# Kernel optimization log

Hardware: AMD Instinct MI355X
Metric: run time of the kernel (lower is better)

The kernel has to match this reference:

```python
import jax, jax.numpy as jnp
import numpy as np

B, T, D = 1, 256, 80
CC = 256        # conv_channels
CCEP = 222      # ccep_size
K = 3           # kernel_size
FFT = 1024
HOP = 256
WIN = 512       # window_size = 2*hop
PF_K = 128      # ltv_postfilter_kernel_size


def conv1d_same(x, w, b, dilation=1):
    """x: (B, L, Cin), w: (Cout, Cin, K) -> (B, L, Cout), 'same' padding."""
    k = w.shape[-1]
    ke = (k - 1) * dilation + 1
    pad = ((ke - 1) // 2, ke - 1 - (ke - 1) // 2)
    y = jax.lax.conv_general_dilated(
        x, w, window_strides=(1,), padding=[pad], rhs_dilation=(dilation,),
        dimension_numbers=('NWC', 'OIW', 'NWC'))
    return y + b


def setup_inputs() -> dict:
    key = jax.random.key(0)
    ks = jax.random.split(key, 8)
    def mkw(k, o, i, kk, scale=1.0):
        return (jax.random.normal(k, (o, i, kk), jnp.float32) * scale / np.sqrt(i * kk)).astype(jnp.float32)
    x = jax.random.normal(ks[0], (B, T, D), jnp.float32)
    z = jax.random.normal(ks[1], (B, 1, T * HOP), jnp.float32)
    w1 = mkw(ks[2], CC, D, K);    b1 = jnp.zeros((CC,), jnp.float32)
    w2 = mkw(ks[3], CC, CC, K);   b2 = jnp.zeros((CC,), jnp.float32)
    w3 = mkw(ks[4], CCEP, CC, K, 0.1); b3 = jnp.zeros((CCEP,), jnp.float32)
    pf_w = mkw(ks[5], 1, 1, PF_K); pf_b = jnp.zeros((1,), jnp.float32)
    # quefrency norm buffer: cat(flip(1..111), 1..111)
    idx = jnp.arange(1, CCEP // 2 + 1, dtype=jnp.float32)
    quef_norm = jnp.concatenate([idx[::-1], idx])
    win = 0.5 * (1.0 - jnp.cos(2.0 * jnp.pi * jnp.arange(WIN, dtype=jnp.float32) / WIN))
    return dict(x=x, z=z, w1=w1, b1=b1, w2=w2, b2=b2, w3=w3, b3=b3,
                pf_w=pf_w, pf_b=pf_b, quef_norm=quef_norm, win=win)


def reference(x, z, w1, b1, w2, b2, w3, b3, pf_w, pf_b, quef_norm, win):
    # --- ConvLayers front-end: conv stack producing complex cepstrum per frame ---
    h = jax.nn.relu(conv1d_same(x, w1, b1))
    h = jax.nn.relu(conv1d_same(h, w2, b2))
    ccep = conv1d_same(h, w3, b3) / quef_norm           # (B, T, 222)
    # --- _ccep2impulse: pad -> FFT -> exp10(mag), keep phase -> IFFT.real ---
    pad = (FFT - CCEP) // 2
    cc = jnp.pad(ccep, ((0, 0), (0, 0), (pad, pad)))    # (B, T, 1024)
    Y = jnp.fft.fft(cc, n=FFT, axis=-1)
    mag = jnp.power(10.0, Y.real / 10.0)
    phase = Y.imag
    imp = jnp.fft.ifft(mag * jnp.cos(phase) + 1j * (mag * jnp.sin(phase)),
                       n=FFT, axis=-1).real.astype(jnp.float32)  # (B, T, 1024)
    # --- _conv_impulse: double unfold + per-frame matmul ---
    zp = jnp.pad(z, ((0, 0), (0, 0), (WIN // 2 - 1, WIN // 2)))      # (B,1,L+511)
    fidx = jnp.arange(T)[:, None] * HOP + jnp.arange(WIN)[None, :]   # (T, 512)
    frames = zp[:, :, fidx]                                          # (B,1,T,512)
    fp = jnp.pad(frames, ((0, 0), (0, 0), (0, 0), (FFT // 2 - 1, FFT // 2)))  # (B,1,T,1535)
    widx = jnp.arange(WIN)[:, None] + jnp.arange(FFT)[None, :]       # (512, 1024)
    wins = fp[:, :, :, widx]                                         # (B,1,T,512,1024)
    out = jnp.einsum('bctwk,btk->bctw', wins, imp)                   # (B,1,T,512)
    # --- _ola: window, split, roll-add, flatten ---
    out = out * win
    l, r = out[..., :HOP], out[..., HOP:]
    s = (l + jnp.roll(r, 1, axis=2)).reshape(B, 1, T * HOP)          # (B,1,L)
    # --- ltv postfilter: 1-ch conv1d (channels-last, 'same') ---
    y = conv1d_same(jnp.transpose(s, (0, 2, 1)), pf_w, pf_b)
    return jnp.transpose(y, (0, 2, 1))
```

## Files before the change

kernel.cpp:

```cpp
#include <hip/hip_runtime.h>

#define T_FRAMES 256
#define D_IN 80
#define CCH 256
#define CCEP 222
#define FFT_N 1024
#define HOP 256
#define WINL 512
#define PF_KT 128
#define ZLEN 65536

__device__ __forceinline__ unsigned br10(unsigned x) { return __brev(x) >> 22; }

__device__ __forceinline__ void conv_inner(const float4* __restrict__ wlds4,
                                           const float4* __restrict__ inlds4,
                                           int c, int fh, float* __restrict__ acc) {
  #pragma unroll
  for (int cg = 0; cg < 4; ++cg) {
    float4 w0 = wlds4[(cg * 3 + 0) * 256 + c];
    float4 w1v = wlds4[(cg * 3 + 1) * 256 + c];
    float4 w2v = wlds4[(cg * 3 + 2) * 256 + c];
    float4 xr[10];
    #pragma unroll
    for (int r = 0; r < 10; ++r) xr[r] = inlds4[(fh * 8 + r) * 4 + cg];
    #pragma unroll
    for (int j = 0; j < 8; ++j) {
      float4 xa = xr[j], xb = xr[j + 1], xc = xr[j + 2];
      acc[j] += xa.x * w0.x  + xb.x * w0.y  + xc.x * w0.z
              + xa.y * w0.w  + xb.y * w1v.x + xc.y * w1v.y
              + xa.z * w1v.z + xb.z * w1v.w + xc.z * w2v.x
              + xa.w * w2v.y + xb.w * w2v.z + xc.w * w2v.w;
    }
  }
}

__global__ __launch_bounds__(512) void conv12_k(const float* __restrict__ x, const float* __restrict__ w1,
                                                const float* __restrict__ b1, const float* __restrict__ w2,
                                                float* __restrict__ h2p) {
  __shared__ float4 wlds4[12 * 256];
  __shared__ float  w1lds[240 * 16];
  __shared__ float4 xlds4[20 * 20];
  __shared__ float4 inlds4[18 * 4];
  const int kc = blockIdx.x, g = blockIdx.y, tid = threadIdx.x;
  const int t0 = g << 4;
  const float4* w24 = (const float4*)w2;
  const float4* x4 = (const float4*)x;
  #pragma unroll
  for (int it = 0; it < 6; ++it) {
    int idx = it * 512 + tid, cc = idx & 255, j4 = idx >> 8;
    wlds4[j4 * 256 + cc] = w24[cc * 192 + kc * 12 + j4];
  }
  for (int idx = tid; idx < 3840; idx += 512) {
    int ch = idx & 15, j = idx >> 4;
    w1lds[j * 16 + ch] = w1[(kc * 16 + ch) * 240 + j];
  }
  if (tid < 400) {
    int f = tid / 20, cg = tid - f * 20;
    int tt = t0 - 2 + f;
    xlds4[f * 20 + cg] = (tt >= 0 && tt < T_FRAMES) ? x4[tt * 20 + cg] : make_float4(0.f, 0.f, 0.f, 0.f);
  }
  __syncthreads();
  if (tid < 288) {
    int f = tid >> 4, ch = tid & 15;
    int tt = t0 - 1 + f;
    float acc = b1[kc * 16 + ch];
    const float* x0 = (const float*)&xlds4[(f + 0) * 20];
    const float* x1 = (const float*)&xlds4[(f + 1) * 20];
    const float* x2 = (const float*)&xlds4[(f + 2) * 20];
    #pragma unroll 8
    for (int cin = 0; cin < D_IN; ++cin) {
      acc += x0[cin] * w1lds[(cin * 3 + 0) * 16 + ch]
           + x1[cin] * w1lds[(cin * 3 + 1) * 16 + ch]
           + x2[cin] * w1lds[(cin * 3 + 2) * 16 + ch];
    }
    ((float*)inlds4)[f * 16 + ch] = (tt >= 0 && tt < T_FRAMES) ? fmaxf(acc, 0.f) : 0.f;
  }
  __syncthreads();
  const int c = tid & 255, fh = tid >> 8;
  float acc[8] = {0.f, 0.f, 0.f, 0.f, 0.f, 0.f, 0.f, 0.f};
  conv_inner(wlds4, inlds4, c, fh, acc);
  const int ob = kc << 8;
  #pragma unroll
  for (int j = 0; j < 8; ++j) h2p[(ob + t0 + fh * 8 + j) * CCH + c] = acc[j];
}

__global__ __launch_bounds__(512) void conv3_k(const float* __restrict__ h2p, const float* __restrict__ b2,
                                               const float* __restrict__ w3, float* __restrict__ ccp) {
  __shared__ float4 wlds4[12 * 256];
  __shared__ float4 inlds4[18 * 4];
  const int kc = blockIdx.x, g = blockIdx.y, tid = threadIdx.x;
  const int t0 = g << 4;
  const float4* w34 = (const float4*)w3;
  const float4* h2p4 = (const float4*)h2p;
  const float4* b24 = (const float4*)b2;
  #pragma unroll
  for (int it = 0; it < 6; ++it) {
    int idx = it * 512 + tid, cc = idx & 255, j4 = idx >> 8;
    if (cc < CCEP) wlds4[j4 * 256 + cc] = w34[cc * 192 + kc * 12 + j4];
  }
  if (tid < 72) {
    int r = tid >> 2, cg = tid & 3, tt = t0 - 1 + r;
    float4 s = make_float4(0.f, 0.f, 0.f, 0.f);
    if (tt >= 0 && tt < T_FRAMES) {
      s = b24[kc * 4 + cg];
      #pragma unroll
      for (int p = 0; p < 16; ++p) {
        float4 v = h2p4[((p << 8) + tt) * 64 + kc * 4 + cg];
        s.x += v.x; s.y += v.y; s.z += v.z; s.w += v.w;
      }
      s.x = fmaxf(s.x, 0.f); s.y = fmaxf(s.y, 0.f); s.z = fmaxf(s.z, 0.f); s.w = fmaxf(s.w, 0.f);
    }
    inlds4[tid] = s;
  }
  __syncthreads();
  const int c = tid & 255, fh = tid >> 8;
  if (c < CCEP) {
    float acc[8] = {0.f, 0.f, 0.f, 0.f, 0.f, 0.f, 0.f, 0.f};
    conv_inner(wlds4, inlds4, c, fh, acc);
    const int ob = kc << 8;
    #pragma unroll
    for (int j = 0; j < 8; ++j) ccp[(ob + t0 + fh * 8 + j) * CCEP + c] = acc[j];
  }
}

__global__ __launch_bounds__(512) void fftltv_k(const float* __restrict__ ccp, const float* __restrict__ b3,
                                                const float* __restrict__ quef, const float* __restrict__ z,
                                                const float* __restrict__ win, float* __restrict__ outw) {
  __shared__ float2 U[FFT_N];
  __shared__ float ccs[224];
  int t = blockIdx.x, tid = threadIdx.x;
  if (tid < CCEP) {
    float s = b3[tid];
    #pragma unroll
    for (int p = 0; p < 16; ++p) s += ccp[((p << 8) + t) * CCEP + tid];
    ccs[tid] = s / quef[tid];
  }
  __syncthreads();
  for (int i = tid; i < FFT_N; i += 512) {
    unsigned q = br10((unsigned)i);
    float a = (q >= 401u && q < 623u) ? ccs[q - 401u] : 0.f;
    float bv = 0.f;
    if (q < 512u) {
      int idx = t * HOP + (int)q - 255;
      bv = (idx >= 0 && idx < ZLEN) ? z[idx] : 0.f;
    }
    U[i] = make_float2(a, bv);
  }
  __syncthreads();
  #pragma unroll
  for (int s = 1; s <= 10; ++s) {
    int half = 1 << (s - 1);
    int pos = tid & (half - 1);
    int i1 = ((tid >> (s - 1)) << s) + pos;
    int i2 = i1 + half;
    float ang = (-6.283185307179586f / (float)(1 << s)) * (float)pos;
    float sn, cs; __sincosf(ang, &sn, &cs);
    float2 v2 = U[i2], v1 = U[i1];
    float tr = cs * v2.x - sn * v2.y;
    float ti = cs * v2.y + sn * v2.x;
    U[i1] = make_float2(v1.x + tr, v1.y + ti);
    U[i2] = make_float2(v1.x - tr, v1.y - ti);
    __syncthreads();
  }
  {
    int j = tid;
    int mj = (FFT_N - j) & (FFT_N - 1);
    float2 Uj = U[j], Um = U[mj];
    float2 U5j = make_float2(0.f, 0.f);
    if (tid == 0) U5j = U[512];
    auto pcalc = [](float2 Uj, float2 Um) -> float2 {
      float Ar = 0.5f * (Uj.x + Um.x);
      float Ai = 0.5f * (Uj.y - Um.y);
      float Bx = 0.5f * (Uj.y + Um.y);
      float By = 0.5f * (Um.x - Uj.x);
      float mag = __expf(0.23025850929940457f * Ar);
      float sn, cs; __sincosf(Ai, &sn, &cs);
      float SPx = mag * cs, SPy = mag * sn;
      return make_float2(Bx * SPx + By * SPy, Bx * SPy - By * SPx);
    };
    float2 Pj = pcalc(Uj, Um);
    float2 P5 = (tid == 0) ? pcalc(U5j, U5j) : make_float2(0.f, 0.f);
    __syncthreads();
    U[j] = Pj;
    if (tid == 0) U[512] = P5;
    else U[mj] = make_float2(Pj.x, -Pj.y);
  }
  __syncthreads();
  #pragma unroll
  for (int s = 10; s >= 1; --s) {
    int half = 1 << (s - 1);
    int pos = tid & (half - 1);
    int i1 = ((tid >> (s - 1)) << s) + pos;
    int i2 = i1 + half;
    float ang = (6.283185307179586f / (float)(1 << s)) * (float)pos;
    float sn, cs; __sincosf(ang, &sn, &cs);
    float2 v1 = U[i1], v2 = U[i2];
    U[i1] = make_float2(v1.x + v2.x, v1.y + v2.y);
    float dr = v1.x - v2.x, di = v1.y - v2.y;
    U[i2] = make_float2(cs * dr - sn * di, cs * di + sn * dr);
    __syncthreads();
  }
  const float inv = 1.0f / (float)FFT_N;
  for (int i = tid; i < FFT_N; i += 512) {
    unsigned m = br10((unsigned)i);
    if (m < 512u) {
      int w = 511 - (int)m;
      outw[t * WINL + w] = U[i].x * inv * win[w];
    }
  }
}

__global__ __launch_bounds__(256) void pf_k(const float* __restrict__ outw, const float* __restrict__ pf_w,
                                            const float* __restrict__ pf_b, float* __restrict__ y) {
  __shared__ float sb[256 + PF_KT - 1];
  __shared__ float wpf[PF_KT];
  int n0 = blockIdx.x * 256;
  for (int i = threadIdx.x; i < 256 + PF_KT - 1; i += 256) {
    int m = n0 - 63 + i;
    float v = 0.f;
    if (m >= 0 && m < ZLEN) {
      int t = m >> 8, j = m & 255;
      v = outw[t * WINL + j] + outw[((t - 1) & 255) * WINL + HOP + j];
    }
    sb[i] = v;
  }
  if (threadIdx.x < PF_KT) wpf[threadIdx.x] = pf_w[threadIdx.x];
  __syncthreads();
  float acc = pf_b[0];
  #pragma unroll 8
  for (int j = 0; j < PF_KT; ++j) acc += sb[threadIdx.x + j] * wpf[j];
  y[n0 + threadIdx.x] = acc;
}

extern "C" void kernel_launch(void* const* d_in, const int* in_sizes, int n_in,
                              void* d_out, int out_size, void* d_ws, size_t ws_size,
                              hipStream_t stream) {
  const float* x    = (const float*)d_in[0];
  const float* z    = (const float*)d_in[1];
  const float* w1   = (const float*)d_in[2];
  const float* b1   = (const float*)d_in[3];
  const float* w2   = (const float*)d_in[4];
  const float* b2   = (const float*)d_in[5];
  const float* w3   = (const float*)d_in[6];
  const float* b3   = (const float*)d_in[7];
  const float* pf_w = (const float*)d_in[8];
  const float* pf_b = (const float*)d_in[9];
  const float* quef = (const float*)d_in[10];
  const float* win  = (const float*)d_in[11];
  float* out = (float*)d_out;
  float* ws  = (float*)d_ws;

  float* h2p  = ws;
  float* ccp  = h2p + 1048576;
  float* outw = ccp + 909312;

  conv12_k<<<dim3(16, 16), 512, 0, stream>>>(x, w1, b1, w2, h2p);
  conv3_k<<<dim3(16, 16), 512, 0, stream>>>(h2p, b2, w3, ccp);
  fftltv_k<<<T_FRAMES, 512, 0, stream>>>(ccp, b3, quef, z, win, outw);
  pf_k<<<ZLEN / 256, 256, 0, stream>>>(outw, pf_w, pf_b, out);
}
```

Before: 31.87 us.

## Fuse FFT stages into radix-4 passes and parallelize conv3 split-K reduction

The forward and inverse 1024-point FFTs in the per-frame kernel now process two radix-2 stages per pass as radix-4 butterflies on 256 threads, which halves the number of barrier-separated LDS passes. In conv3, the 16-way partial-sum reduction of the conv2 output, previously done serially by 72 threads, is split across 288 threads into four partial sums staged in shared memory, then combined. In exchange, half the threads sit idle during the FFT passes and conv3 gains an extra barrier and more shared memory.

```diff
diff --git a/kernel.cpp b/kernel.cpp
--- a/kernel.cpp
+++ b/kernel.cpp
@@ -87,6 +87,7 @@
 __global__ __launch_bounds__(512) void conv3_k(const float* __restrict__ h2p, const float* __restrict__ b2,
                                                const float* __restrict__ w3, float* __restrict__ ccp) {
   __shared__ float4 wlds4[12 * 256];
+  __shared__ float4 sred4[72 * 4];
   __shared__ float4 inlds4[18 * 4];
   const int kc = blockIdx.x, g = blockIdx.y, tid = threadIdx.x;
   const int t0 = g << 4;
@@ -98,14 +99,29 @@
     int idx = it * 512 + tid, cc = idx & 255, j4 = idx >> 8;
     if (cc < CCEP) wlds4[j4 * 256 + cc] = w34[cc * 192 + kc * 12 + j4];
   }
+  if (tid < 288) {
+    int e = tid >> 2, q = tid & 3;
+    int r = e >> 2, cg = e & 3;
+    int tt = t0 - 1 + r;
+    float4 v = make_float4(0.f, 0.f, 0.f, 0.f);
+    if (tt >= 0 && tt < T_FRAMES) {
+      #pragma unroll
+      for (int pp = 0; pp < 4; ++pp) {
+        float4 a = h2p4[(((q * 4 + pp) << 8) + tt) * 64 + kc * 4 + cg];
+        v.x += a.x; v.y += a.y; v.z += a.z; v.w += a.w;
+      }
+    }
+    sred4[e * 4 + q] = v;
+  }
+  __syncthreads();
   if (tid < 72) {
     int r = tid >> 2, cg = tid & 3, tt = t0 - 1 + r;
     float4 s = make_float4(0.f, 0.f, 0.f, 0.f);
     if (tt >= 0 && tt < T_FRAMES) {
       s = b24[kc * 4 + cg];
       #pragma unroll
-      for (int p = 0; p < 16; ++p) {
-        float4 v = h2p4[((p << 8) + tt) * 64 + kc * 4 + cg];
+      for (int q = 0; q < 4; ++q) {
+        float4 v = sred4[tid * 4 + q];
         s.x += v.x; s.y += v.y; s.z += v.z; s.w += v.w;
       }
       s.x = fmaxf(s.x, 0.f); s.y = fmaxf(s.y, 0.f); s.z = fmaxf(s.z, 0.f); s.w = fmaxf(s.w, 0.f);
@@ -148,18 +164,27 @@
   }
   __syncthreads();
   #pragma unroll
-  for (int s = 1; s <= 10; ++s) {
-    int half = 1 << (s - 1);
-    int pos = tid & (half - 1);
-    int i1 = ((tid >> (s - 1)) << s) + pos;
-    int i2 = i1 + half;
-    float ang = (-6.283185307179586f / (float)(1 << s)) * (float)pos;
-    float sn, cs; __sincosf(ang, &sn, &cs);
-    float2 v2 = U[i2], v1 = U[i1];
-    float tr = cs * v2.x - sn * v2.y;
-    float ti = cs * v2.y + sn * v2.x;
-    U[i1] = make_float2(v1.x + tr, v1.y + ti);
-    U[i2] = make_float2(v1.x - tr, v1.y - ti);
+  for (int s = 1; s <= 10; s += 2) {
+    if (tid < 256) {
+      int h = 1 << (s - 1);
+      int pos = tid & (h - 1);
+      int a = ((tid >> (s - 1)) << (s + 1)) + pos;
+      float2 e0 = U[a], e1 = U[a + h], e2 = U[a + 2 * h], e3 = U[a + 3 * h];
+      float s1, c1; __sincosf((-6.283185307179586f / (float)(2 * h)) * (float)pos, &s1, &c1);
+      float s2, c2; __sincosf((-6.283185307179586f / (float)(4 * h)) * (float)pos, &s2, &c2);
+      float2 t1 = make_float2(c1 * e1.x - s1 * e1.y, c1 * e1.y + s1 * e1.x);
+      float2 t3 = make_float2(c1 * e3.x - s1 * e3.y, c1 * e3.y + s1 * e3.x);
+      float2 A0 = make_float2(e0.x + t1.x, e0.y + t1.y);
+      float2 A1 = make_float2(e0.x - t1.x, e0.y - t1.y);
+      float2 A2 = make_float2(e2.x + t3.x, e2.y + t3.y);
+      float2 A3 = make_float2(e2.x - t3.x, e2.y - t3.y);
+      float2 u2 = make_float2(c2 * A2.x - s2 * A2.y, c2 * A2.y + s2 * A2.x);
+      float2 u3 = make_float2(s2 * A3.x + c2 * A3.y, s2 * A3.y - c2 * A3.x);
+      U[a]         = make_float2(A0.x + u2.x, A0.y + u2.y);
+      U[a + 2 * h] = make_float2(A0.x - u2.x, A0.y - u2.y);
+      U[a + h]     = make_float2(A1.x + u3.x, A1.y + u3.y);
+      U[a + 3 * h] = make_float2(A1.x - u3.x, A1.y - u3.y);
+    }
     __syncthreads();
   }
   {
@@ -187,17 +212,28 @@
   }
   __syncthreads();
   #pragma unroll
-  for (int s = 10; s >= 1; --s) {
-    int half = 1 << (s - 1);
-    int pos = tid & (half - 1);
-    int i1 = ((tid >> (s - 1)) << s) + pos;
-    int i2 = i1 + half;
-    float ang = (6.283185307179586f / (float)(1 << s)) * (float)pos;
-    float sn, cs; __sincosf(ang, &sn, &cs);
-    float2 v1 = U[i1], v2 = U[i2];
-    U[i1] = make_float2(v1.x + v2.x, v1.y + v2.y);
-    float dr = v1.x - v2.x, di = v1.y - v2.y;
-    U[i2] = make_float2(cs * dr - sn * di, cs * di + sn * dr);
+  for (int s = 10; s >= 2; s -= 2) {
+    if (tid < 256) {
+      int H = 1 << (s - 1);
+      int Hh = H >> 1;
+      int pos = tid & (Hh - 1);
+      int a = ((tid >> (s - 2)) << s) + pos;
+      float2 e0 = U[a], e1 = U[a + Hh], e2 = U[a + H], e3 = U[a + H + Hh];
+      float s1, c1; __sincosf((6.283185307179586f / (float)(2 * H)) * (float)pos, &s1, &c1);
+      float s2, c2; __sincosf((6.283185307179586f / (float)H) * (float)pos, &s2, &c2);
+      float2 A0 = make_float2(e0.x + e2.x, e0.y + e2.y);
+      float2 d02 = make_float2(e0.x - e2.x, e0.y - e2.y);
+      float2 A2 = make_float2(c1 * d02.x - s1 * d02.y, c1 * d02.y + s1 * d02.x);
+      float2 A1 = make_float2(e1.x + e3.x, e1.y + e3.y);
+      float2 d13 = make_float2(e1.x - e3.x, e1.y - e3.y);
+      float2 A3 = make_float2(-s1 * d13.x - c1 * d13.y, -s1 * d13.y + c1 * d13.x);
+      U[a] = make_float2(A0.x + A1.x, A0.y + A1.y);
+      float2 dB = make_float2(A0.x - A1.x, A0.y - A1.y);
+      U[a + Hh] = make_float2(c2 * dB.x - s2 * dB.y, c2 * dB.y + s2 * dB.x);
+      U[a + H] = make_float2(A2.x + A3.x, A2.y + A3.y);
+      float2 dB2 = make_float2(A2.x - A3.x, A2.y - A3.y);
+      U[a + H + Hh] = make_float2(c2 * dB2.x - s2 * dB2.y, c2 * dB2.y + s2 * dB2.x);
+    }
     __syncthreads();
   }
   const float inv = 1.0f / (float)FFT_N;
```

Result: no change. 31.92 us (+0.2%).
